# Kernel tuning notes

Measured on AMD Instinct MI355X. Metric: run time of the kernel, lower is better.

The kernel has to match this reference:

```python
import jax, jax.numpy as jnp
import numpy as np

C = 256

def setup_inputs() -> dict:
    key = jax.random.key(0)
    ks = jax.random.split(key, 9)
    B, H, W = 32, 32, 32
    s = C ** -0.5  # init scale for weights
    inputs = jax.random.normal(ks[0], (B, H, W, C), jnp.float32)
    Wq = jax.random.normal(ks[1], (C, C), jnp.float32) * s
    Wk = jax.random.normal(ks[2], (C, C), jnp.float32) * s
    Wv = jax.random.normal(ks[3], (C, C), jnp.float32) * s
    Wo = jax.random.normal(ks[4], (C, C), jnp.float32) * s
    bq = jnp.zeros((C,), jnp.float32)
    bk = jnp.zeros((C,), jnp.float32)
    bv = jnp.zeros((C,), jnp.float32)
    bo = jnp.zeros((C,), jnp.float32)
    return {"inputs": inputs, "Wq": Wq, "bq": bq, "Wk": Wk, "bk": bk,
            "Wv": Wv, "bv": bv, "Wo": Wo, "bo": bo}

def reference(inputs, Wq, bq, Wk, bk, Wv, bv, Wo, bo):
    B, H, W, c = inputs.shape
    scale = jnp.float32(c) ** -0.5
    x = inputs.reshape(B, H * W, c)           # 1x1 conv == per-pixel matmul
    q = x @ Wq + bq                           # [B, HW, C]
    k = x @ Wk + bk
    v = x @ Wv + bv
    scores = jnp.einsum('bnc,bmc->bnm', q, k) * scale  # [B, HW, HW]
    attn = jax.nn.softmax(scores, axis=-1)
    attended = jnp.einsum('bnm,bmc->bnc', attn, v)     # [B, HW, C]
    out = attended @ Wo + bo
    return out.reshape(B, H, W, c)
```

## Files before the change

### kernel.cpp

```cpp
#include <hip/hip_runtime.h>
#include <hip/hip_bf16.h>

typedef __bf16 bf16;
typedef __bf16 bf16x2 __attribute__((ext_vector_type(2)));
typedef __bf16 bf16x4 __attribute__((ext_vector_type(4)));
typedef __bf16 bf16x8 __attribute__((ext_vector_type(8)));
typedef float f32x4 __attribute__((ext_vector_type(4)));

#define SM_C 0.09016994374947424f

typedef __attribute__((address_space(1))) const void as1_void;
typedef __attribute__((address_space(3))) void as3_void;

__global__ __launch_bounds__(256) void transpose_w(
    const float* __restrict__ Wq, const float* __restrict__ Wk,
    const float* __restrict__ Wv, const float* __restrict__ Wo,
    bf16* __restrict__ Wt)
{
    __shared__ float T[32][33];
    const int bid = blockIdx.x;
    const int m = bid >> 6, tile = bid & 63;
    const int tn0 = (tile >> 3) * 32, tk0 = (tile & 7) * 32;
    const float* W = (m == 0) ? Wq : (m == 1) ? Wk : (m == 2) ? Wv : Wo;

    const int t = threadIdx.x;
    const int r = t >> 3, c4 = (t & 7) * 4;

    f32x4 v = *(const f32x4*)(W + (size_t)(tk0 + r) * 256 + tn0 + c4);
#pragma unroll
    for (int j = 0; j < 4; ++j) T[r][c4 + j] = v[j];
    __syncthreads();

    bf16x4 ov;
#pragma unroll
    for (int j = 0; j < 4; ++j) ov[j] = (bf16)T[c4 + j][r];
    *(bf16x4*)(Wt + (size_t)m * 65536 + (size_t)(tn0 + r) * 256 + tk0 + c4) = ov;
}

__global__ __launch_bounds__(256, 3) void qkv_gemm(
    const float* __restrict__ X, const bf16* __restrict__ Wt,
    const float* __restrict__ bq, const float* __restrict__ bk,
    const float* __restrict__ bv,
    bf16* __restrict__ Qo, bf16* __restrict__ Ko, bf16* __restrict__ Vto)
{
    __shared__ __align__(16) char qsmem[36864];
    bf16* const Xs  = (bf16*)qsmem;
    bf16* const Ws_ = (bf16*)(qsmem + 18432);
    bf16* const Cs  = (bf16*)qsmem;

    const int t    = threadIdx.x;
    const int lane = t & 63, wv = t >> 6;
    const int quad = lane >> 4, l16 = lane & 15;
    const int bm   = blockIdx.x;
    const int bn   = blockIdx.y;
    const int proj = bn >> 1;

    const bf16* W = Wt + (size_t)proj * 65536 + (size_t)(bn & 1) * 32768;
    const float* bias = (proj == 0) ? bq : (proj == 1) ? bk : bv;

    const int m0 = t >> 3;
    const int c0 = (t & 7) * 8;

    const f32x4 zero = {0.0f, 0.0f, 0.0f, 0.0f};
    f32x4 acc[2][8];
#pragma unroll
    for (int i = 0; i < 2; ++i)
#pragma unroll
        for (int j = 0; j < 8; ++j) acc[i][j] = zero;

    f32x4 xa[4], xb[4]; bf16x8 wp[4];
#pragma unroll
    for (int p = 0; p < 4; ++p) {
        const float* px = X + (size_t)(bm * 128 + m0 + p * 32) * 256 + c0;
        xa[p] = *(const f32x4*)px; xb[p] = *(const f32x4*)(px + 4);
        wp[p] = *(const bf16x8*)(W + (size_t)(m0 + p * 32) * 256 + c0);
    }

    for (int kt = 0; kt < 4; ++kt) {
#pragma unroll
        for (int p = 0; p < 4; ++p) {
            bf16x8 r;
#pragma unroll
            for (int j = 0; j < 4; ++j) { r[j] = (bf16)xa[p][j]; r[j + 4] = (bf16)xb[p][j]; }
            *(bf16x8*)(Xs + (m0 + p * 32) * 72 + c0) = r;
            *(bf16x8*)(Ws_ + (m0 + p * 32) * 72 + c0) = wp[p];
        }
        __syncthreads();

        if (kt < 3) {
#pragma unroll
            for (int p = 0; p < 4; ++p) {
                const float* px = X + (size_t)(bm * 128 + m0 + p * 32) * 256 + (kt + 1) * 64 + c0;
                xa[p] = *(const f32x4*)px; xb[p] = *(const f32x4*)(px + 4);
                wp[p] = *(const bf16x8*)(W + (size_t)(m0 + p * 32) * 256 + (kt + 1) * 64 + c0);
            }
        }

#pragma unroll
        for (int ks = 0; ks < 2; ++ks) {
            bf16x8 a[2], bb[8];
#pragma unroll
            for (int mt = 0; mt < 2; ++mt)
                a[mt] = *(const bf16x8*)(Xs + (wv * 32 + mt * 16 + l16) * 72 + ks * 32 + quad * 8);
#pragma unroll
            for (int nt = 0; nt < 8; ++nt)
                bb[nt] = *(const bf16x8*)(Ws_ + (nt * 16 + l16) * 72 + ks * 32 + quad * 8);
#pragma unroll
            for (int mt = 0; mt < 2; ++mt)
#pragma unroll
                for (int nt = 0; nt < 8; ++nt)
                    acc[mt][nt] = __builtin_amdgcn_mfma_f32_16x16x32_bf16(
                        a[mt], bb[nt], acc[mt][nt], 0, 0, 0);
        }
        __syncthreads();
    }

    if (proj == 2) {
#pragma unroll
        for (int nt = 0; nt < 8; ++nt) {
            int col = (bn & 1) * 128 + nt * 16 + l16;
            float bvv = bias[col];
#pragma unroll
            for (int mt = 0; mt < 2; ++mt) {
                int grow0 = bm * 128 + wv * 32 + mt * 16 + quad * 4;
                bf16x4 pk;
#pragma unroll
                for (int r = 0; r < 4; ++r) pk[r] = (bf16)(acc[mt][nt][r] + bvv);
                int b = grow0 >> 10, m = grow0 & 1023;
                *(bf16x4*)(Vto + (size_t)b * 262144 + (size_t)col * 1024 + m) = pk;
            }
        }
    } else {
        bf16* dst = (proj == 0) ? Qo : Ko;
#pragma unroll
        for (int nt = 0; nt < 8; ++nt) {
            float bvv = bias[(bn & 1) * 128 + nt * 16 + l16];
#pragma unroll
            for (int mt = 0; mt < 2; ++mt)
#pragma unroll
                for (int r = 0; r < 4; ++r)
                    Cs[(wv * 32 + mt * 16 + quad * 4 + r) * 132 + nt * 16 + l16] =
                        (bf16)(acc[mt][nt][r] + bvv);
        }
        __syncthreads();
#pragma unroll
        for (int i = 0; i < 8; ++i) {
            int chunk = i * 256 + t;
            int row = chunk >> 4, cc = chunk & 15;
            bf16x8 v = *(const bf16x8*)(Cs + row * 132 + cc * 8);
            *(bf16x8*)(dst + (size_t)(bm * 128 + row) * 256 + (bn & 1) * 128 + cc * 8) = v;
        }
    }
}

__global__ __launch_bounds__(256, 2) void flash_attn(
    const bf16* __restrict__ Qr, const bf16* __restrict__ K,
    const bf16* __restrict__ Vt, const bf16* __restrict__ Wo,
    const float* __restrict__ bo, float* __restrict__ out)
{
    __shared__ __align__(16) char smem[81920];

    const int t    = threadIdx.x;
    const int lane = t & 63, wv = t >> 6;
    const int quad = lane >> 4, l16 = lane & 15;
    const int b  = blockIdx.x;
    const int qt = blockIdx.y;

    bf16x8 qf[2][8];
#pragma unroll
    for (int mt = 0; mt < 2; ++mt) {
        const bf16* qp = Qr + ((size_t)b * 1024 + qt * 128 + wv * 32 + mt * 16 + l16) * 256 + quad * 8;
#pragma unroll
        for (int ks = 0; ks < 8; ++ks)
            qf[mt][ks] = *(const bf16x8*)(qp + ks * 32);
    }

    const f32x4 zero = {0.0f, 0.0f, 0.0f, 0.0f};
    f32x4 o[2][16];
#pragma unroll
    for (int mt = 0; mt < 2; ++mt)
#pragma unroll
        for (int n = 0; n < 16; ++n) o[mt][n] = zero;
    float lst[2] = {0.f, 0.f};

    auto gloadK = [&](int T, int buf) {
#pragma unroll
        for (int p = 0; p < 4; ++p) {
            int chunk = wv * 4 + p;
            int row   = chunk * 2 + (lane >> 5);
            int s     = (lane & 31) ^ (row & 7);
            const bf16* gsrc = K + ((size_t)b * 1024 + T * 32 + row) * 256 + s * 8;
            __builtin_amdgcn_global_load_lds((as1_void*)gsrc,
                (as3_void*)(smem + buf * 16384 + chunk * 1024), 16, 0, 0);
        }
    };
    auto gloadV = [&](int T, int buf) {
#pragma unroll
        for (int p = 0; p < 4; ++p) {
            int chunk = wv * 4 + p;
            int row   = chunk * 16 + (lane >> 2);
            int s     = (lane & 3) ^ (row & 3);
            const bf16* gsrc = Vt + (size_t)b * 262144 + (size_t)row * 1024 + T * 32 + s * 8;
            __builtin_amdgcn_global_load_lds((as1_void*)gsrc,
                (as3_void*)(smem + 32768 + buf * 16384 + chunk * 1024), 16, 0, 0);
        }
    };

    char* const Pb = smem + 65536 + wv * 1024;
    const int psw = (l16 & 7) << 4;

    gloadK(0, 0); gloadV(0, 0);

    for (int j = 0; j < 32; ++j) {
        const int buf = j & 1;
        __syncthreads();

        if (j < 31) { gloadK(j + 1, buf ^ 1); gloadV(j + 1, buf ^ 1); }

        f32x4 s2[2][2];
        s2[0][0] = zero; s2[0][1] = zero; s2[1][0] = zero; s2[1][1] = zero;
        const char* Kb = smem + buf * 16384;
#pragma unroll
        for (int ks = 0; ks < 8; ++ks) {
#pragma unroll
            for (int n = 0; n < 2; ++n) {
                bf16x8 kb = *(const bf16x8*)(Kb + (n * 16 + l16) * 512 +
                                             (((ks * 4 + quad) ^ (l16 & 7)) << 4));
                s2[0][n] = __builtin_amdgcn_mfma_f32_16x16x32_bf16(kb, qf[0][ks], s2[0][n], 0, 0, 0);
                s2[1][n] = __builtin_amdgcn_mfma_f32_16x16x32_bf16(kb, qf[1][ks], s2[1][n], 0, 0, 0);
            }
        }

        bf16x8 af[2];
#pragma unroll
        for (int mt = 0; mt < 2; ++mt) {
#pragma unroll
            for (int n = 0; n < 2; ++n) {
#pragma unroll
                for (int h = 0; h < 2; ++h) {
                    float p0 = __builtin_amdgcn_exp2f(s2[mt][n][2 * h] * SM_C);
                    float p1 = __builtin_amdgcn_exp2f(s2[mt][n][2 * h + 1] * SM_C);
                    lst[mt] += p0 + p1;
                    bf16x2 pk; pk[0] = (bf16)p0; pk[1] = (bf16)p1;
                    *(bf16x2*)(Pb + ((l16 * 64 + n * 32 + quad * 8 + h * 4) ^ psw)) = pk;
                }
            }
            af[mt] = *(const bf16x8*)(Pb + ((l16 * 64 + quad * 16) ^ psw));
        }

        const char* Vb = smem + 32768 + buf * 16384;
#pragma unroll
        for (int n = 0; n < 16; ++n) {
            bf16x8 vb = *(const bf16x8*)(Vb + (n * 16 + l16) * 64 +
                                         ((quad ^ (l16 & 3)) << 4));
            o[0][n] = __builtin_amdgcn_mfma_f32_16x16x32_bf16(af[0], vb, o[0][n], 0, 0, 0);
            o[1][n] = __builtin_amdgcn_mfma_f32_16x16x32_bf16(af[1], vb, o[1][n], 0, 0, 0);
        }
    }

    __syncthreads();

#pragma unroll
    for (int mt = 0; mt < 2; ++mt) {
        lst[mt] += __shfl_xor(lst[mt], 16, 64);
        lst[mt] += __shfl_xor(lst[mt], 32, 64);
    }
    float inv[2][4];
#pragma unroll
    for (int mt = 0; mt < 2; ++mt)
#pragma unroll
        for (int r = 0; r < 4; ++r)
            inv[mt][r] = 1.0f / __shfl(lst[mt], quad * 4 + r, 64);

#pragma unroll
    for (int mt = 0; mt < 2; ++mt)
#pragma unroll
        for (int n = 0; n < 16; ++n)
#pragma unroll
            for (int r = 0; r < 4; ++r) {
                int row = wv * 32 + mt * 16 + quad * 4 + r;
                int col = n * 16 + l16;
                *(bf16*)(smem + row * 512 + ((col * 2) ^ ((row & 7) << 4))) =
                    (bf16)(o[mt][n][r] * inv[mt][r]);
            }

    const size_t orow0 = (size_t)b * 1024 + qt * 128 + wv * 32;
    for (int sl = 0; sl < 8; ++sl) {
        __syncthreads();
#pragma unroll
        for (int p = 0; p < 4; ++p) {
            int chunk = wv * 4 + p;
            int row   = chunk * 2 + (lane >> 5);
            int s     = (lane & 31) ^ (row & 7);
            const bf16* gsrc = Wo + (size_t)(sl * 32 + row) * 256 + s * 8;
            __builtin_amdgcn_global_load_lds((as1_void*)gsrc,
                (as3_void*)(smem + 65536 + chunk * 1024), 16, 0, 0);
        }
        __syncthreads();

        f32x4 acc[2][2];
        acc[0][0] = zero; acc[0][1] = zero; acc[1][0] = zero; acc[1][1] = zero;
#pragma unroll
        for (int ks = 0; ks < 8; ++ks) {
            bf16x8 a[2], bb[2];
#pragma unroll
            for (int rt = 0; rt < 2; ++rt) {
                int row = wv * 32 + rt * 16 + l16;
                a[rt] = *(const bf16x8*)(smem + row * 512 +
                                         (((ks * 4 + quad) ^ (l16 & 7)) << 4));
            }
#pragma unroll
            for (int ct = 0; ct < 2; ++ct) {
                int row = ct * 16 + l16;
                bb[ct] = *(const bf16x8*)(smem + 65536 + row * 512 +
                                          (((ks * 4 + quad) ^ (l16 & 7)) << 4));
            }
#pragma unroll
            for (int rt = 0; rt < 2; ++rt)
#pragma unroll
                for (int ct = 0; ct < 2; ++ct)
                    acc[rt][ct] = __builtin_amdgcn_mfma_f32_16x16x32_bf16(
                        a[rt], bb[ct], acc[rt][ct], 0, 0, 0);
        }

#pragma unroll
        for (int ct = 0; ct < 2; ++ct) {
            int col = sl * 32 + ct * 16 + l16;
            float bvv = bo[col];
#pragma unroll
            for (int rt = 0; rt < 2; ++rt)
#pragma unroll
                for (int r = 0; r < 4; ++r) {
                    size_t row = orow0 + rt * 16 + quad * 4 + r;
                    out[row * 256 + col] = acc[rt][ct][r] + bvv;
                }
        }
    }
}

extern "C" void kernel_launch(void* const* d_in, const int* in_sizes, int n_in,
                              void* d_out, int out_size, void* d_ws, size_t ws_size,
                              hipStream_t stream)
{
    (void)in_sizes; (void)n_in; (void)out_size; (void)ws_size;
    const float* X  = (const float*)d_in[0];
    const float* Wq = (const float*)d_in[1];
    const float* bq = (const float*)d_in[2];
    const float* Wk = (const float*)d_in[3];
    const float* bk = (const float*)d_in[4];
    const float* Wv = (const float*)d_in[5];
    const float* bv = (const float*)d_in[6];
    const float* Wo = (const float*)d_in[7];
    const float* bo = (const float*)d_in[8];
    float* out = (float*)d_out;

    const size_t NTOK = (size_t)32768 * 256;

    bf16* Wt  = (bf16*)d_ws;
    bf16* Qw  = (bf16*)d_ws + 262144;
    bf16* Kw  = Qw + NTOK;
    bf16* Vtw = Kw + NTOK;

    transpose_w<<<256, 256, 0, stream>>>(Wq, Wk, Wv, Wo, Wt);
    qkv_gemm   <<<dim3(256, 6), 256, 0, stream>>>(X, Wt, bq, bk, bv, Qw, Kw, Vtw);
    flash_attn <<<dim3(32, 8),  256, 0, stream>>>(Qw, Kw, Vtw, Wt + 3 * 65536, bo, out);
}
```

Baseline: 187.3 us.

## Switch flash attention to 32x32x16 MFMA with 8 waves splitting output channels

Rewrites the attention kernel so each block runs 512 threads, with 4 query groups times 2 channel halves. The QK^T and PV products move to 32x32x16 MFMA instructions. P is rearranged in registers via cross-half-wave shuffles instead of going through an LDS scratch buffer. The output projection also uses 32x32 MFMA with 64-column Wo slices. The aim is fewer instructions, less LDS traffic and more waves per block, but each channel-half wave now recomputes the full QK^T scores, duplicating that work, and LDS use rises to 96KB.

```diff
diff --git a/kernel.cpp b/kernel.cpp
--- a/kernel.cpp
+++ b/kernel.cpp
@@ -6,6 +6,8 @@
 typedef __bf16 bf16x4 __attribute__((ext_vector_type(4)));
 typedef __bf16 bf16x8 __attribute__((ext_vector_type(8)));
 typedef float f32x4 __attribute__((ext_vector_type(4)));
+typedef float f32x16 __attribute__((ext_vector_type(16)));
+typedef unsigned int u32;
 
 #define SM_C 0.09016994374947424f
 
@@ -153,61 +155,59 @@
     }
 }
 
-__global__ __launch_bounds__(256, 2) void flash_attn(
+__global__ __launch_bounds__(512, 2) void flash_attn(
     const bf16* __restrict__ Qr, const bf16* __restrict__ K,
     const bf16* __restrict__ Vt, const bf16* __restrict__ Wo,
     const float* __restrict__ bo, float* __restrict__ out)
 {
-    __shared__ __align__(16) char smem[81920];
+    __shared__ __align__(16) char smem[98304];
 
     const int t    = threadIdx.x;
     const int lane = t & 63, wv = t >> 6;
-    const int quad = lane >> 4, l16 = lane & 15;
+    const int l32  = lane & 31, hi = lane >> 5;
+    const int qg   = wv & 3, cg = wv >> 2;
     const int b  = blockIdx.x;
     const int qt = blockIdx.y;
 
-    bf16x8 qf[2][8];
-#pragma unroll
-    for (int mt = 0; mt < 2; ++mt) {
-        const bf16* qp = Qr + ((size_t)b * 1024 + qt * 128 + wv * 32 + mt * 16 + l16) * 256 + quad * 8;
-#pragma unroll
-        for (int ks = 0; ks < 8; ++ks)
-            qf[mt][ks] = *(const bf16x8*)(qp + ks * 32);
-    }
-
-    const f32x4 zero = {0.0f, 0.0f, 0.0f, 0.0f};
-    f32x4 o[2][16];
-#pragma unroll
-    for (int mt = 0; mt < 2; ++mt)
-#pragma unroll
-        for (int n = 0; n < 16; ++n) o[mt][n] = zero;
-    float lst[2] = {0.f, 0.f};
+    bf16x8 qf[16];
+    {
+        const bf16* qp = Qr + ((size_t)b * 1024 + qt * 128 + qg * 32 + l32) * 256 + hi * 8;
+#pragma unroll
+        for (int ks = 0; ks < 16; ++ks)
+            qf[ks] = *(const bf16x8*)(qp + ks * 16);
+    }
+
+    f32x16 o[4];
+#pragma unroll
+    for (int n = 0; n < 4; ++n)
+#pragma unroll
+        for (int i = 0; i < 16; ++i) o[n][i] = 0.0f;
+    float lst = 0.f;
 
     auto gloadK = [&](int T, int buf) {
 #pragma unroll
-        for (int p = 0; p < 4; ++p) {
-            int chunk = wv * 4 + p;
-            int row   = chunk * 2 + (lane >> 5);
-            int s     = (lane & 31) ^ (row & 7);
-            const bf16* gsrc = K + ((size_t)b * 1024 + T * 32 + row) * 256 + s * 8;
-            __builtin_amdgcn_global_load_lds((as1_void*)gsrc,
+        for (int p = 0; p < 2; ++p) {
+            int chunk = wv * 2 + p;
+            int S = chunk * 64 + lane;
+            int kv = S >> 5, sp = S & 31;
+            int ss = sp ^ (kv & 7);
+            const bf16* g = K + ((size_t)b * 1024 + T * 32 + kv) * 256 + ss * 8;
+            __builtin_amdgcn_global_load_lds((as1_void*)g,
                 (as3_void*)(smem + buf * 16384 + chunk * 1024), 16, 0, 0);
         }
     };
     auto gloadV = [&](int T, int buf) {
 #pragma unroll
-        for (int p = 0; p < 4; ++p) {
-            int chunk = wv * 4 + p;
-            int row   = chunk * 16 + (lane >> 2);
-            int s     = (lane & 3) ^ (row & 3);
-            const bf16* gsrc = Vt + (size_t)b * 262144 + (size_t)row * 1024 + T * 32 + s * 8;
-            __builtin_amdgcn_global_load_lds((as1_void*)gsrc,
+        for (int p = 0; p < 2; ++p) {
+            int chunk = wv * 2 + p;
+            int S = chunk * 64 + lane;
+            int ch = S >> 2, sp = S & 3;
+            int ss = sp ^ (ch & 3);
+            const bf16* g = Vt + (size_t)b * 262144 + (size_t)ch * 1024 + T * 32 + ss * 8;
+            __builtin_amdgcn_global_load_lds((as1_void*)g,
                 (as3_void*)(smem + 32768 + buf * 16384 + chunk * 1024), 16, 0, 0);
         }
     };
-
-    char* const Pb = smem + 65536 + wv * 1024;
-    const int psw = (l16 & 7) << 4;
 
     gloadK(0, 0); gloadV(0, 0);
 
@@ -217,123 +217,119 @@
 
         if (j < 31) { gloadK(j + 1, buf ^ 1); gloadV(j + 1, buf ^ 1); }
 
-        f32x4 s2[2][2];
-        s2[0][0] = zero; s2[0][1] = zero; s2[1][0] = zero; s2[1][1] = zero;
+        f32x16 s;
+#pragma unroll
+        for (int i = 0; i < 16; ++i) s[i] = 0.0f;
         const char* Kb = smem + buf * 16384;
 #pragma unroll
-        for (int ks = 0; ks < 8; ++ks) {
-#pragma unroll
-            for (int n = 0; n < 2; ++n) {
-                bf16x8 kb = *(const bf16x8*)(Kb + (n * 16 + l16) * 512 +
-                                             (((ks * 4 + quad) ^ (l16 & 7)) << 4));
-                s2[0][n] = __builtin_amdgcn_mfma_f32_16x16x32_bf16(kb, qf[0][ks], s2[0][n], 0, 0, 0);
-                s2[1][n] = __builtin_amdgcn_mfma_f32_16x16x32_bf16(kb, qf[1][ks], s2[1][n], 0, 0, 0);
-            }
-        }
-
-        bf16x8 af[2];
-#pragma unroll
-        for (int mt = 0; mt < 2; ++mt) {
-#pragma unroll
-            for (int n = 0; n < 2; ++n) {
-#pragma unroll
-                for (int h = 0; h < 2; ++h) {
-                    float p0 = __builtin_amdgcn_exp2f(s2[mt][n][2 * h] * SM_C);
-                    float p1 = __builtin_amdgcn_exp2f(s2[mt][n][2 * h + 1] * SM_C);
-                    lst[mt] += p0 + p1;
-                    bf16x2 pk; pk[0] = (bf16)p0; pk[1] = (bf16)p1;
-                    *(bf16x2*)(Pb + ((l16 * 64 + n * 32 + quad * 8 + h * 4) ^ psw)) = pk;
-                }
-            }
-            af[mt] = *(const bf16x8*)(Pb + ((l16 * 64 + quad * 16) ^ psw));
-        }
+        for (int ks = 0; ks < 16; ++ks) {
+            int ss = (ks * 2 + hi) ^ (l32 & 7);
+            bf16x8 kb = *(const bf16x8*)(Kb + l32 * 512 + ss * 16);
+            s = __builtin_amdgcn_mfma_f32_32x32x16_bf16(kb, qf[ks], s, 0, 0, 0);
+        }
+
+        float p[16];
+#pragma unroll
+        for (int r = 0; r < 16; ++r) { p[r] = __builtin_amdgcn_exp2f(s[r] * SM_C); lst += p[r]; }
+
+        u32 w[8];
+#pragma unroll
+        for (int i = 0; i < 8; ++i) {
+            bf16x2 v2; v2[0] = (bf16)p[2 * i]; v2[1] = (bf16)p[2 * i + 1];
+            w[i] = __builtin_bit_cast(u32, v2);
+        }
+        u32 s0 = hi ? w[0] : w[2];
+        u32 s1 = hi ? w[1] : w[3];
+        u32 r0 = (u32)__shfl_xor((int)s0, 32, 64);
+        u32 r1 = (u32)__shfl_xor((int)s1, 32, 64);
+        u32 s2 = hi ? w[4] : w[6];
+        u32 s3 = hi ? w[5] : w[7];
+        u32 r2 = (u32)__shfl_xor((int)s2, 32, 64);
+        u32 r3 = (u32)__shfl_xor((int)s3, 32, 64);
+        u32 f0[4], f1[4];
+        f0[0] = hi ? r0 : w[0];  f0[1] = hi ? r1 : w[1];
+        f0[2] = hi ? w[2] : r0;  f0[3] = hi ? w[3] : r1;
+        f1[0] = hi ? r2 : w[4];  f1[1] = hi ? r3 : w[5];
+        f1[2] = hi ? w[6] : r2;  f1[3] = hi ? w[7] : r3;
+        bf16x8 pa0, pa1;
+        __builtin_memcpy(&pa0, f0, 16);
+        __builtin_memcpy(&pa1, f1, 16);
 
         const char* Vb = smem + 32768 + buf * 16384;
 #pragma unroll
-        for (int n = 0; n < 16; ++n) {
-            bf16x8 vb = *(const bf16x8*)(Vb + (n * 16 + l16) * 64 +
-                                         ((quad ^ (l16 & 3)) << 4));
-            o[0][n] = __builtin_amdgcn_mfma_f32_16x16x32_bf16(af[0], vb, o[0][n], 0, 0, 0);
-            o[1][n] = __builtin_amdgcn_mfma_f32_16x16x32_bf16(af[1], vb, o[1][n], 0, 0, 0);
+        for (int n = 0; n < 4; ++n) {
+            int chb = cg * 128 + n * 32 + l32;
+            const char* vrow = Vb + chb * 64;
+            bf16x8 v0 = *(const bf16x8*)(vrow + ((hi ^ (chb & 3)) << 4));
+            bf16x8 v1 = *(const bf16x8*)(vrow + (((2 + hi) ^ (chb & 3)) << 4));
+            o[n] = __builtin_amdgcn_mfma_f32_32x32x16_bf16(pa0, v0, o[n], 0, 0, 0);
+            o[n] = __builtin_amdgcn_mfma_f32_32x32x16_bf16(pa1, v1, o[n], 0, 0, 0);
         }
     }
 
     __syncthreads();
 
-#pragma unroll
-    for (int mt = 0; mt < 2; ++mt) {
-        lst[mt] += __shfl_xor(lst[mt], 16, 64);
-        lst[mt] += __shfl_xor(lst[mt], 32, 64);
-    }
-    float inv[2][4];
-#pragma unroll
-    for (int mt = 0; mt < 2; ++mt)
-#pragma unroll
-        for (int r = 0; r < 4; ++r)
-            inv[mt][r] = 1.0f / __shfl(lst[mt], quad * 4 + r, 64);
-
-#pragma unroll
-    for (int mt = 0; mt < 2; ++mt)
-#pragma unroll
-        for (int n = 0; n < 16; ++n)
-#pragma unroll
-            for (int r = 0; r < 4; ++r) {
-                int row = wv * 32 + mt * 16 + quad * 4 + r;
-                int col = n * 16 + l16;
-                *(bf16*)(smem + row * 512 + ((col * 2) ^ ((row & 7) << 4))) =
-                    (bf16)(o[mt][n][r] * inv[mt][r]);
-            }
-
-    const size_t orow0 = (size_t)b * 1024 + qt * 128 + wv * 32;
-    for (int sl = 0; sl < 8; ++sl) {
-        __syncthreads();
+    auto gloadW = [&](int sl) {
 #pragma unroll
         for (int p = 0; p < 4; ++p) {
             int chunk = wv * 4 + p;
-            int row   = chunk * 2 + (lane >> 5);
-            int s     = (lane & 31) ^ (row & 7);
-            const bf16* gsrc = Wo + (size_t)(sl * 32 + row) * 256 + s * 8;
-            __builtin_amdgcn_global_load_lds((as1_void*)gsrc,
+            int S = chunk * 64 + lane;
+            int row = S >> 5, sp = S & 31;
+            int ss = sp ^ (row & 7);
+            const bf16* g = Wo + (size_t)(sl * 64 + row) * 256 + ss * 8;
+            __builtin_amdgcn_global_load_lds((as1_void*)g,
                 (as3_void*)(smem + 65536 + chunk * 1024), 16, 0, 0);
         }
-        __syncthreads();
-
-        f32x4 acc[2][2];
-        acc[0][0] = zero; acc[0][1] = zero; acc[1][0] = zero; acc[1][1] = zero;
-#pragma unroll
-        for (int ks = 0; ks < 8; ++ks) {
-            bf16x8 a[2], bb[2];
-#pragma unroll
-            for (int rt = 0; rt < 2; ++rt) {
-                int row = wv * 32 + rt * 16 + l16;
-                a[rt] = *(const bf16x8*)(smem + row * 512 +
-                                         (((ks * 4 + quad) ^ (l16 & 7)) << 4));
-            }
-#pragma unroll
-            for (int ct = 0; ct < 2; ++ct) {
-                int row = ct * 16 + l16;
-                bb[ct] = *(const bf16x8*)(smem + 65536 + row * 512 +
-                                          (((ks * 4 + quad) ^ (l16 & 7)) << 4));
-            }
-#pragma unroll
-            for (int rt = 0; rt < 2; ++rt)
-#pragma unroll
-                for (int ct = 0; ct < 2; ++ct)
-                    acc[rt][ct] = __builtin_amdgcn_mfma_f32_16x16x32_bf16(
-                        a[rt], bb[ct], acc[rt][ct], 0, 0, 0);
-        }
-
-#pragma unroll
-        for (int ct = 0; ct < 2; ++ct) {
-            int col = sl * 32 + ct * 16 + l16;
-            float bvv = bo[col];
-#pragma unroll
-            for (int rt = 0; rt < 2; ++rt)
-#pragma unroll
-                for (int r = 0; r < 4; ++r) {
-                    size_t row = orow0 + rt * 16 + quad * 4 + r;
-                    out[row * 256 + col] = acc[rt][ct][r] + bvv;
-                }
+    };
+    gloadW(0);
+
+    lst += __shfl_xor(lst, 32, 64);
+    float inv = 1.0f / lst;
+    float invr[16];
+#pragma unroll
+    for (int r = 0; r < 16; ++r)
+        invr[r] = __shfl(inv, (r & 3) + 8 * (r >> 2) + 4 * hi, 64);
+
+#pragma unroll
+    for (int n = 0; n < 4; ++n) {
+        int ch = cg * 128 + n * 32 + l32;
+        int sl16 = ch >> 3, cb = (ch & 7) * 2;
+#pragma unroll
+        for (int r = 0; r < 16; ++r) {
+            int q = qg * 32 + (r & 3) + 8 * (r >> 2) + 4 * hi;
+            *(bf16*)(smem + q * 512 + ((sl16 ^ (q & 7)) << 4) + cb) =
+                (bf16)(o[n][r] * invr[r]);
+        }
+    }
+    __syncthreads();
+
+    const size_t orow0 = (size_t)b * 1024 + qt * 128;
+    for (int sl = 0; sl < 4; ++sl) {
+        f32x16 acc;
+#pragma unroll
+        for (int i = 0; i < 16; ++i) acc[i] = 0.0f;
+        const int q = qg * 32 + l32;
+        const int wr = cg * 32 + l32;
+#pragma unroll
+        for (int ks = 0; ks < 16; ++ks) {
+            int sb = ks * 2 + hi;
+            bf16x8 a  = *(const bf16x8*)(smem + q * 512 + ((sb ^ (q & 7)) << 4));
+            bf16x8 bb = *(const bf16x8*)(smem + 65536 + wr * 512 + ((sb ^ (wr & 7)) << 4));
+            acc = __builtin_amdgcn_mfma_f32_32x32x16_bf16(a, bb, acc, 0, 0, 0);
+        }
+
+        int col = sl * 64 + cg * 32 + l32;
+        float bvv = bo[col];
+#pragma unroll
+        for (int r = 0; r < 16; ++r) {
+            int qq = qg * 32 + (r & 3) + 8 * (r >> 2) + 4 * hi;
+            out[(orow0 + qq) * 256 + col] = acc[r] + bvv;
+        }
+
+        if (sl < 3) {
+            __syncthreads();
+            gloadW(sl + 1);
+            __syncthreads();
         }
     }
 }
@@ -363,5 +359,5 @@
 
     transpose_w<<<256, 256, 0, stream>>>(Wq, Wk, Wv, Wo, Wt);
     qkv_gemm   <<<dim3(256, 6), 256, 0, stream>>>(X, Wt, bq, bk, bv, Qw, Kw, Vtw);
-    flash_attn <<<dim3(32, 8),  256, 0, stream>>>(Qw, Kw, Vtw, Wt + 3 * 65536, bo, out);
+    flash_attn <<<dim3(32, 8), 512, 0, stream>>>(Qw, Kw, Vtw, Wt + 3 * 65536, bo, out);
 }
```

Result: no change. 185.8 us (-0.8%).
